# Optimization experiments

Measured on AMD Instinct MI355X. Metric: run time of the kernel, lower is better.

The kernel has to match this reference:

```python
import jax, jax.numpy as jnp
import numpy as np

B, N, D, H = 256, 40, 256, 256      # molecules, atoms/molecule, pc_hidden, pred_hidden
nS, nC, nB = 40, 5, 5               # n_SYMBOLS, n_FORMAL_CHARGES, n_BOND_TYPES
NEG_SLOPE = 0.01                    # F.leaky_relu default


def _lrelu(x):
    return jnp.where(x >= 0, x, NEG_SLOPE * x)


def setup_inputs() -> dict:
    key = jax.random.key(0)
    ks = jax.random.split(key, 7)
    def w(k, shape, fan_in):
        return jax.random.normal(k, shape, jnp.float32) / np.float32(np.sqrt(fan_in))
    return {
        "yhat": jax.random.normal(ks[0], (B, N, D), jnp.float32),
        "Ws1": w(ks[1], (D, H), D),      "bs1": jnp.zeros((H,), jnp.float32),
        "Ws2": w(ks[2], (H, nS), H),     "bs2": jnp.zeros((nS,), jnp.float32),
        "Wc1": w(ks[3], (D, H), D),      "bc1": jnp.zeros((H,), jnp.float32),
        "Wc2": w(ks[4], (H, nC), H),     "bc2": jnp.zeros((nC,), jnp.float32),
        "Wb1": w(ks[5], (2 * D, H), 2 * D), "bb1": jnp.zeros((H,), jnp.float32),
        "Wb2": w(ks[6], (H, nB), H),     "bb2": jnp.zeros((nB,), jnp.float32),
    }


def reference(yhat, Ws1, bs1, Ws2, bs2, Wc1, bc1, Wc2, bc2, Wb1, bb1, Wb2, bb2):
    # Per-atom symbol / charge heads (2-layer MLP with leaky_relu)
    symbols = _lrelu(yhat @ Ws1 + bs1) @ Ws2 + bs2          # [B, N, nS]
    charges = _lrelu(yhat @ Wc1 + bc1) @ Wc2 + bc2          # [B, N, nC]

    # Pairwise bond head: concat(x_i, x_j) @ Wb1 == x_i @ Wb1[:D] + x_j @ Wb1[D:]
    # (avoids materializing the [B, N, N, 2D] concat tensor)
    p1 = yhat @ Wb1[:D]                                      # [B, N, H]
    p2 = yhat @ Wb1[D:]                                      # [B, N, H]
    h = _lrelu(p1[:, :, None, :] + p2[:, None, :, :] + bb1)  # [B, N, N, H]
    bonds = h @ Wb2 + bb2                                    # [B, N, N, nB]
    bonds = bonds + jnp.swapaxes(bonds, 1, 2)                # symmetrize (i,j)+(j,i)

    return (symbols.reshape(-1, nS),
            charges.reshape(-1, nC),
            bonds.reshape(-1, nB))
```

## Files before the change

kernel.cpp:

```cpp
#include <hip/hip_runtime.h>
#include <hip/hip_bf16.h>

typedef unsigned short u16;
typedef __attribute__((ext_vector_type(4))) int   int4v;
typedef __attribute__((ext_vector_type(4))) unsigned int uint4v;
typedef __attribute__((ext_vector_type(4))) unsigned short ushort4v;
typedef __attribute__((ext_vector_type(4))) float floatx4;
typedef __attribute__((ext_vector_type(8))) short bf16x8;
typedef _Float16 half8 __attribute__((ext_vector_type(8)));
typedef _Float16 half2v __attribute__((ext_vector_type(2)));

#define LRELU_NS 0.01f
#define SK 264

__device__ __forceinline__ float bitsToF(unsigned int b) {
    union { unsigned int u; float f; } v; v.u = b << 16; return v.f;
}
__device__ __forceinline__ u16 f2bf(float f) {
    __hip_bfloat16 h = __float2bfloat16(f);
    return *reinterpret_cast<u16*>(&h);
}
__device__ __forceinline__ float lrelu(float v) {
    return fmaxf(v, LRELU_NS * v);
}
__device__ __forceinline__ u16 ldW(const void* p, int i, int isF32) {
    return isF32 ? f2bf(((const float*)p)[i]) : ((const u16*)p)[i];
}
__device__ __forceinline__ float ldF(const void* p, int i, int isF32) {
    return isF32 ? ((const float*)p)[i]
                 : bitsToF((unsigned int)((const u16*)p)[i]);
}
__device__ __forceinline__ u16 f2h_bits(float f) {
    union { _Float16 h; u16 u; } v; v.h = (_Float16)f; return v.u;
}
__device__ __forceinline__ u16 ldWh(const void* p, int i, int isF32) {
    float f = isF32 ? ((const float*)p)[i]
                    : bitsToF((unsigned int)((const u16*)p)[i]);
    return f2h_bits(f);
}
__device__ __forceinline__ half2v u2h2(unsigned int x) {
    union { unsigned int u; half2v h; } v; v.u = x; return v.h;
}
__device__ __forceinline__ unsigned int h22u(half2v x) {
    union { half2v h; unsigned int u; } v; v.h = x; return v.u;
}

__device__ __forceinline__ int computeIsF32(const u16* y, int* cnt, int t) {
    if (t == 0) *cnt = 0;
    __syncthreads();
    if (t < 256) {
        u16 v = y[2 * t];
        int e = (v >> 7) & 0xFF;
        if (v == 0 || (e >= 96 && e < 160)) atomicAdd(cnt, 1);
    }
    __syncthreads();
    return (*cnt < 192) ? 1 : 0;
}

__global__ __launch_bounds__(256) void pack_kernel(
    const void* __restrict__ yhat,
    const void* __restrict__ Ws1, const void* __restrict__ Wc1,
    const void* __restrict__ Wb1, const void* __restrict__ Ws2,
    const void* __restrict__ Wc2,
    const void* __restrict__ bs1, const void* __restrict__ bc1,
    const void* __restrict__ bb1, const void* __restrict__ bs2,
    const void* __restrict__ bc2, const void* __restrict__ bb2,
    u16* __restrict__ WallT, u16* __restrict__ W2T, float* __restrict__ biasF)
{
    __shared__ int fcnt;
    const int bid = blockIdx.x, t = threadIdx.x;
    const int isF32 = computeIsF32((const u16*)yhat, &fcnt, t);
    if (bid < 64) {
        __shared__ u16 tile[64][65];
        const int c0 = (bid & 15) * 64;
        const int k0 = (bid >> 4) * 64;
        const void* src; int coff; int roff = 0;
        if (c0 < 256)      { src = Ws1; coff = c0; }
        else if (c0 < 512) { src = Wc1; coff = c0 - 256; }
        else if (c0 < 768) { src = Wb1; coff = c0 - 512; }
        else               { src = Wb1; coff = c0 - 768; roff = 256; }
        const int cc = t & 63, kk0 = t >> 6;
        #pragma unroll
        for (int i = 0; i < 16; ++i) {
            int kk = kk0 + i * 4;
            tile[kk][cc] = ldW(src, (k0 + kk + roff) * 256 + coff + cc, isF32);
        }
        __syncthreads();
        const int kk2 = t & 63, cc0 = t >> 6;
        #pragma unroll
        for (int i = 0; i < 16; ++i) {
            int cc2 = cc0 + i * 4;
            WallT[(c0 + cc2) * 256 + (k0 + kk2)] = tile[kk2][cc2];
        }
    } else if (bid < 128) {
        int e2 = (bid - 64) * 256 + t;
        int c = e2 >> 8, k = e2 & 255;
        u16 v = 0;
        if (c < 40)                 v = ldW(Ws2, k * 40 + c, isF32);
        else if (c >= 48 && c < 53) v = ldW(Wc2, k * 5 + (c - 48), isF32);
        W2T[c * 256 + k] = v;
    } else {
        int idx = (bid - 128) * 256 + t;
        float v = 0.f;
        if (idx < 256)       v = ldF(bs1, idx, isF32);
        else if (idx < 512)  v = ldF(bc1, idx - 256, isF32);
        else if (idx < 768)  v = ldF(bb1, idx - 512, isF32);
        else if (idx < 808)  v = ldF(bs2, idx - 768, isF32);
        else if (idx < 813)  v = ldF(bc2, idx - 808, isF32);
        else if (idx >= 816 && idx < 821) v = ldF(bb2, idx - 816, isF32);
        biasF[idx] = v;
    }
}

union SharedHB {
    struct { u16 Xs[64 * SK]; u16 Hb[64 * SK]; } hd;
    struct { u16 Xm[48 * SK]; u16 P1L[48 * SK]; u16 P2L[48 * SK];
             u16 WsB[5 * 264]; } bd;
};

__global__ __launch_bounds__(512) void fused_kernel(
    const void* __restrict__ Xv, const u16* __restrict__ WallT,
    const u16* __restrict__ W2T, const void* __restrict__ Wb2,
    const float* __restrict__ biasF, void* __restrict__ outv)
{
    __shared__ SharedHB sh;
    __shared__ int fcnt;
    const int t = threadIdx.x;
    const int bid = blockIdx.x;
    const int isF32 = computeIsF32((const u16*)Xv, &fcnt, t);

    const int w = t >> 6, l = t & 63;
    const int ml = l & 15, kq = l >> 4, r0 = kq * 4;

    if (bid < 512) {
        const int b = bid >> 1;
        const int h = bid & 1;

        if (isF32) {
            const floatx4* __restrict__ src = (const floatx4*)((const float*)Xv + b * 10240);
            #pragma unroll
            for (int s = 0; s < 5; ++s) {
                int cid = t + s * 512;
                int row = cid >> 6, ch = cid & 63;
                floatx4 f = src[cid];
                ushort4v u;
                u[0] = f2bf(f[0]); u[1] = f2bf(f[1]); u[2] = f2bf(f[2]); u[3] = f2bf(f[3]);
                *(ushort4v*)&sh.bd.Xm[row * SK + ch * 4] = u;
            }
            {
                int row = 40 + (t >> 6), ch = t & 63;
                ushort4v z = {0, 0, 0, 0};
                *(ushort4v*)&sh.bd.Xm[row * SK + ch * 4] = z;
            }
        } else {
            const int4v* __restrict__ src = (const int4v*)((const u16*)Xv + b * 10240);
            #pragma unroll
            for (int s = 0; s < 3; ++s) {
                int cid = t + s * 512;
                int row = cid >> 5, ch = cid & 31;
                if (cid < 1280) *(int4v*)&sh.bd.Xm[row * SK + ch * 8] = src[cid];
                else { int4v z = {0, 0, 0, 0}; *(int4v*)&sh.bd.Xm[row * SK + ch * 8] = z; }
            }
        }
        #pragma unroll
        for (int s = 0; s < 3; ++s) {
            int e2 = t + s * 512;
            if (e2 < 1280) {
                int c = e2 >> 8, k = e2 & 255;
                sh.bd.WsB[c * 264 + k] = ldWh(Wb2, k * 5 + c, isF32);
            }
        }
        __syncthreads();

        for (int n = 0; n < 4; ++n) {
            const int gc = (w + 8 * n) * 16 + ml;
            floatx4 acc[3] = {};
            #pragma unroll
            for (int ks = 0; ks < 8; ++ks) {
                const int k0 = ks * 32 + kq * 8;
                bf16x8 bf = *(const bf16x8*)&WallT[(512 + gc) * 256 + k0];
                #pragma unroll
                for (int i = 0; i < 3; ++i) {
                    bf16x8 a = *(const bf16x8*)&sh.bd.Xm[(i * 16 + ml) * SK + k0];
                    acc[i] = __builtin_amdgcn_mfma_f32_16x16x32_bf16(a, bf, acc[i], 0, 0, 0);
                }
            }
            u16* dst = (gc < 256) ? sh.bd.P1L : sh.bd.P2L;
            const int col = gc & 255;
            const float bias = (gc < 256) ? biasF[512 + gc] : 0.f;
            #pragma unroll
            for (int i = 0; i < 3; ++i)
                #pragma unroll
                for (int r = 0; r < 4; ++r)
                    dst[(i * 16 + r0 + r) * SK + col] = f2h_bits(acc[i][r] + bias);
        }
        __syncthreads();

        const int sel = (ml < 5) ? ml : 4;
        half8 wf[8];
        #pragma unroll
        for (int ks = 0; ks < 8; ++ks)
            wf[ks] = *(const half8*)&sh.bd.WsB[sel * 264 + ks * 32 + kq * 8];
        const float b2x2 = 2.f * biasF[816 + ml];
        const _Float16 c001 = (_Float16)0.01f;

        constexpr int mT[11]  = {0, 0, 0, 1, 1, 1, 2, 2, 3, 3, 4};
        constexpr int jtT[11] = {0, 1, 2, 0, 1, 2, 1, 2, 1, 2, 2};
        #pragma unroll
        for (int idx = 0; idx < 11; ++idx) {
            if ((idx & 1) != h) continue;
            const int m = mT[idx], jt = jtT[idx];
            const int i = w + 8 * m;
            const bool diag = (jt == (i >> 4));
            floatx4 acc = {};
            #pragma unroll
            for (int ks = 0; ks < 8; ++ks) {
                const int k0 = ks * 32 + kq * 8;
                const uint4v a1 = *(const uint4v*)&sh.bd.P1L[i * SK + k0];
                const uint4v a2 = *(const uint4v*)&sh.bd.P2L[i * SK + k0];
                const uint4v b1 = *(const uint4v*)&sh.bd.P1L[(jt * 16 + ml) * SK + k0];
                const uint4v b2 = *(const uint4v*)&sh.bd.P2L[(jt * 16 + ml) * SK + k0];
                union { unsigned int u[4]; half8 v; } af;
                #pragma unroll
                for (int d = 0; d < 4; ++d) {
                    const half2v tF = u2h2(a1[d]) + u2h2(b2[d]);
                    const half2v tB = u2h2(b1[d]) + u2h2(a2[d]);
                    const half2v lF = __builtin_elementwise_max(tF, tF * c001);
                    const half2v lB = __builtin_elementwise_max(tB, tB * c001);
                    af.u[d] = h22u(lF + lB);
                }
                acc = __builtin_amdgcn_mfma_f32_16x16x32_f16(af.v, wf[ks], acc, 0, 0, 0);
            }
            if (ml < 5) {
                #pragma unroll
                for (int r = 0; r < 4; ++r) {
                    const int j = jt * 16 + r0 + r;
                    if (j < 40 && (!diag || j >= i)) {
                        const float v = acc[r] + b2x2;
                        const int o1 = 460800 + (b * 1600 + i * 40 + j) * 5 + ml;
                        if (isF32) ((float*)outv)[o1] = v;
                        else ((__hip_bfloat16*)outv)[o1] = __float2bfloat16(v);
                        if (!diag || j > i) {
                            const int o2 = 460800 + (b * 1600 + j * 40 + i) * 5 + ml;
                            if (isF32) ((float*)outv)[o2] = v;
                            else ((__hip_bfloat16*)outv)[o2] = __float2bfloat16(v);
                        }
                    }
                }
            }
        }
    } else {
        const int hb = bid - 512;
        const int bm0 = (hb % 160) * 64;
        const int head = hb / 160;

        if (isF32) {
            const floatx4* __restrict__ src = (const floatx4*)((const float*)Xv + bm0 * 256);
            #pragma unroll
            for (int s = 0; s < 8; ++s) {
                int cid = t + s * 512;
                int row = cid >> 6, ch = cid & 63;
                floatx4 f = src[cid];
                ushort4v u;
                u[0] = f2bf(f[0]); u[1] = f2bf(f[1]); u[2] = f2bf(f[2]); u[3] = f2bf(f[3]);
                *(ushort4v*)&sh.hd.Xs[row * SK + ch * 4] = u;
            }
        } else {
            const int4v* __restrict__ src = (const int4v*)((const u16*)Xv + bm0 * 256);
            #pragma unroll
            for (int s = 0; s < 4; ++s) {
                int cid = t + s * 512;
                int row = cid >> 5, ch = cid & 31;
                *(int4v*)&sh.hd.Xs[row * SK + ch * 8] = src[cid];
            }
        }
        __syncthreads();

        #pragma unroll
        for (int n = 0; n < 2; ++n) {
            const int ct = w + 8 * n;
            floatx4 acc[4] = {};
            #pragma unroll
            for (int ks = 0; ks < 8; ++ks) {
                const int k0 = ks * 32 + kq * 8;
                bf16x8 bf = *(const bf16x8*)&WallT[(head * 256 + ct * 16 + ml) * 256 + k0];
                #pragma unroll
                for (int mt = 0; mt < 4; ++mt) {
                    bf16x8 a = *(const bf16x8*)&sh.hd.Xs[(mt * 16 + ml) * SK + k0];
                    acc[mt] = __builtin_amdgcn_mfma_f32_16x16x32_bf16(a, bf, acc[mt], 0, 0, 0);
                }
            }
            const int col = ct * 16 + ml;
            const float bias = biasF[head * 256 + col];
            #pragma unroll
            for (int mt = 0; mt < 4; ++mt)
                #pragma unroll
                for (int r = 0; r < 4; ++r)
                    sh.hd.Hb[(mt * 16 + r0 + r) * SK + col] = f2bf(lrelu(acc[mt][r] + bias));
        }
        __syncthreads();

        if (w < 4) {
            const int nct = (head == 0) ? 3 : 1;
            const int c0  = (head == 0) ? 0 : 48;
            floatx4 acc2[3] = {};
            #pragma unroll
            for (int ks = 0; ks < 8; ++ks) {
                const int k0 = ks * 32 + kq * 8;
                bf16x8 a = *(const bf16x8*)&sh.hd.Hb[(w * 16 + ml) * SK + k0];
                #pragma unroll
                for (int j = 0; j < 3; ++j) {
                    if (j < nct) {
                        bf16x8 bf = *(const bf16x8*)&W2T[(c0 + j * 16 + ml) * 256 + k0];
                        acc2[j] = __builtin_amdgcn_mfma_f32_16x16x32_bf16(a, bf, acc2[j], 0, 0, 0);
                    }
                }
            }
            #pragma unroll
            for (int j = 0; j < 3; ++j) {
                if (j < nct) {
                    const int col = j * 16 + ml;
                    const int lim = (head == 0) ? 40 : 5;
                    if (col < lim) {
                        const float bias = biasF[(head == 0 ? 768 : 808) + col];
                        #pragma unroll
                        for (int r = 0; r < 4; ++r) {
                            const int row = bm0 + w * 16 + r0 + r;
                            const int o = (head == 0) ? row * 40 + col
                                                      : 409600 + row * 5 + col;
                            const float v = acc2[j][r] + bias;
                            if (isF32) ((float*)outv)[o] = v;
                            else ((__hip_bfloat16*)outv)[o] = __float2bfloat16(v);
                        }
                    }
                }
            }
        }
    }
}

extern "C" void kernel_launch(void* const* d_in, const int* in_sizes, int n_in,
                              void* d_out, int out_size, void* d_ws, size_t ws_size,
                              hipStream_t stream)
{
    const void* yhat = d_in[0];
    const void* Ws1  = d_in[1];
    const void* bs1  = d_in[2];
    const void* Ws2  = d_in[3];
    const void* bs2  = d_in[4];
    const void* Wc1  = d_in[5];
    const void* bc1  = d_in[6];
    const void* Wc2  = d_in[7];
    const void* bc2  = d_in[8];
    const void* Wb1  = d_in[9];
    const void* bb1  = d_in[10];
    const void* Wb2  = d_in[11];
    const void* bb2  = d_in[12];

    char* wsb = (char*)d_ws;
    float* biasF = (float*)(wsb + 4096);
    u16*   W2T   = (u16*)(wsb + 8192);
    u16*   WallT = (u16*)(wsb + 40960);

    pack_kernel<<<132, 256, 0, stream>>>(yhat, Ws1, Wc1, Wb1, Ws2, Wc2,
                                         bs1, bc1, bb1, bs2, bc2, bb2,
                                         WallT, W2T, biasF);
    fused_kernel<<<832, 512, 0, stream>>>(yhat, WallT, W2T, Wb2, biasF, d_out);
}
```

Before: 133.8 us.

## Alias LDS buffers across phases to shrink shared memory and raise occupancy

Overlays the input tile with the P1/hidden buffers in shared memory. The MFMA results are held in packed registers, a barrier is inserted, and only then are they written into the aliased region. This reduces LDS per block (the bond path drops from about 3 tiles to 2, the heads path from 2 to 1), so more workgroups can be resident per CU, and launch_bounds now requests 6. The cost is an extra __syncthreads per path and more live registers, which could cause spills under the tighter register budget.

```diff
diff --git a/kernel.cpp b/kernel.cpp
--- a/kernel.cpp
+++ b/kernel.cpp
@@ -113,12 +113,17 @@
 }
 
 union SharedHB {
-    struct { u16 Xs[64 * SK]; u16 Hb[64 * SK]; } hd;
-    struct { u16 Xm[48 * SK]; u16 P1L[48 * SK]; u16 P2L[48 * SK];
-             u16 WsB[5 * 264]; } bd;
+    struct {
+        union { u16 Xm[48 * SK]; u16 P1L[48 * SK]; } a;
+        u16 P2L[48 * SK];
+        u16 WsB[5 * 264];
+    } bd;
+    struct {
+        union { u16 Xs[64 * SK]; u16 Hb[64 * SK]; } x;
+    } hd;
 };
 
-__global__ __launch_bounds__(512) void fused_kernel(
+__global__ __launch_bounds__(512, 6) void fused_kernel(
     const void* __restrict__ Xv, const u16* __restrict__ WallT,
     const u16* __restrict__ W2T, const void* __restrict__ Wb2,
     const float* __restrict__ biasF, void* __restrict__ outv)
@@ -145,12 +150,12 @@
                 floatx4 f = src[cid];
                 ushort4v u;
                 u[0] = f2bf(f[0]); u[1] = f2bf(f[1]); u[2] = f2bf(f[2]); u[3] = f2bf(f[3]);
-                *(ushort4v*)&sh.bd.Xm[row * SK + ch * 4] = u;
+                *(ushort4v*)&sh.bd.a.Xm[row * SK + ch * 4] = u;
             }
             {
                 int row = 40 + (t >> 6), ch = t & 63;
                 ushort4v z = {0, 0, 0, 0};
-                *(ushort4v*)&sh.bd.Xm[row * SK + ch * 4] = z;
+                *(ushort4v*)&sh.bd.a.Xm[row * SK + ch * 4] = z;
             }
         } else {
             const int4v* __restrict__ src = (const int4v*)((const u16*)Xv + b * 10240);
@@ -158,8 +163,8 @@
             for (int s = 0; s < 3; ++s) {
                 int cid = t + s * 512;
                 int row = cid >> 5, ch = cid & 31;
-                if (cid < 1280) *(int4v*)&sh.bd.Xm[row * SK + ch * 8] = src[cid];
-                else { int4v z = {0, 0, 0, 0}; *(int4v*)&sh.bd.Xm[row * SK + ch * 8] = z; }
+                if (cid < 1280) *(int4v*)&sh.bd.a.Xm[row * SK + ch * 8] = src[cid];
+                else { int4v z = {0, 0, 0, 0}; *(int4v*)&sh.bd.a.Xm[row * SK + ch * 8] = z; }
             }
         }
         #pragma unroll
@@ -172,6 +177,8 @@
         }
         __syncthreads();
 
+        unsigned int pH[24];
+        #pragma unroll
         for (int n = 0; n < 4; ++n) {
             const int gc = (w + 8 * n) * 16 + ml;
             floatx4 acc[3] = {};
@@ -181,18 +188,37 @@
                 bf16x8 bf = *(const bf16x8*)&WallT[(512 + gc) * 256 + k0];
                 #pragma unroll
                 for (int i = 0; i < 3; ++i) {
-                    bf16x8 a = *(const bf16x8*)&sh.bd.Xm[(i * 16 + ml) * SK + k0];
+                    bf16x8 a = *(const bf16x8*)&sh.bd.a.Xm[(i * 16 + ml) * SK + k0];
                     acc[i] = __builtin_amdgcn_mfma_f32_16x16x32_bf16(a, bf, acc[i], 0, 0, 0);
                 }
             }
-            u16* dst = (gc < 256) ? sh.bd.P1L : sh.bd.P2L;
+            const float bias = (gc < 256) ? biasF[512 + gc] : 0.f;
+            #pragma unroll
+            for (int i = 0; i < 3; ++i) {
+                const unsigned int h0 = f2h_bits(acc[i][0] + bias);
+                const unsigned int h1 = f2h_bits(acc[i][1] + bias);
+                const unsigned int h2 = f2h_bits(acc[i][2] + bias);
+                const unsigned int h3 = f2h_bits(acc[i][3] + bias);
+                pH[n * 6 + i * 2 + 0] = h0 | (h1 << 16);
+                pH[n * 6 + i * 2 + 1] = h2 | (h3 << 16);
+            }
+        }
+        __syncthreads();
+
+        #pragma unroll
+        for (int n = 0; n < 4; ++n) {
+            const int gc = (w + 8 * n) * 16 + ml;
+            u16* dst = (gc < 256) ? sh.bd.a.P1L : sh.bd.P2L;
             const int col = gc & 255;
-            const float bias = (gc < 256) ? biasF[512 + gc] : 0.f;
-            #pragma unroll
-            for (int i = 0; i < 3; ++i)
-                #pragma unroll
-                for (int r = 0; r < 4; ++r)
-                    dst[(i * 16 + r0 + r) * SK + col] = f2h_bits(acc[i][r] + bias);
+            #pragma unroll
+            for (int i = 0; i < 3; ++i) {
+                const unsigned int p0 = pH[n * 6 + i * 2 + 0];
+                const unsigned int p1 = pH[n * 6 + i * 2 + 1];
+                dst[(i * 16 + r0 + 0) * SK + col] = (u16)(p0 & 0xffff);
+                dst[(i * 16 + r0 + 1) * SK + col] = (u16)(p0 >> 16);
+                dst[(i * 16 + r0 + 2) * SK + col] = (u16)(p1 & 0xffff);
+                dst[(i * 16 + r0 + 3) * SK + col] = (u16)(p1 >> 16);
+            }
         }
         __syncthreads();
 
@@ -216,9 +242,9 @@
             #pragma unroll
             for (int ks = 0; ks < 8; ++ks) {
                 const int k0 = ks * 32 + kq * 8;
-                const uint4v a1 = *(const uint4v*)&sh.bd.P1L[i * SK + k0];
+                const uint4v a1 = *(const uint4v*)&sh.bd.a.P1L[i * SK + k0];
                 const uint4v a2 = *(const uint4v*)&sh.bd.P2L[i * SK + k0];
-                const uint4v b1 = *(const uint4v*)&sh.bd.P1L[(jt * 16 + ml) * SK + k0];
+                const uint4v b1 = *(const uint4v*)&sh.bd.a.P1L[(jt * 16 + ml) * SK + k0];
                 const uint4v b2 = *(const uint4v*)&sh.bd.P2L[(jt * 16 + ml) * SK + k0];
                 union { unsigned int u[4]; half8 v; } af;
                 #pragma unroll
@@ -263,7 +289,7 @@
                 floatx4 f = src[cid];
                 ushort4v u;
                 u[0] = f2bf(f[0]); u[1] = f2bf(f[1]); u[2] = f2bf(f[2]); u[3] = f2bf(f[3]);
-                *(ushort4v*)&sh.hd.Xs[row * SK + ch * 4] = u;
+                *(ushort4v*)&sh.hd.x.Xs[row * SK + ch * 4] = u;
             }
         } else {
             const int4v* __restrict__ src = (const int4v*)((const u16*)Xv + bm0 * 256);
@@ -271,11 +297,12 @@
             for (int s = 0; s < 4; ++s) {
                 int cid = t + s * 512;
                 int row = cid >> 5, ch = cid & 31;
-                *(int4v*)&sh.hd.Xs[row * SK + ch * 8] = src[cid];
-            }
-        }
-        __syncthreads();
-
+                *(int4v*)&sh.hd.x.Xs[row * SK + ch * 8] = src[cid];
+            }
+        }
+        __syncthreads();
+
+        unsigned int hH[16];
         #pragma unroll
         for (int n = 0; n < 2; ++n) {
             const int ct = w + 8 * n;
@@ -286,17 +313,36 @@
                 bf16x8 bf = *(const bf16x8*)&WallT[(head * 256 + ct * 16 + ml) * 256 + k0];
                 #pragma unroll
                 for (int mt = 0; mt < 4; ++mt) {
-                    bf16x8 a = *(const bf16x8*)&sh.hd.Xs[(mt * 16 + ml) * SK + k0];
+                    bf16x8 a = *(const bf16x8*)&sh.hd.x.Xs[(mt * 16 + ml) * SK + k0];
                     acc[mt] = __builtin_amdgcn_mfma_f32_16x16x32_bf16(a, bf, acc[mt], 0, 0, 0);
                 }
             }
             const int col = ct * 16 + ml;
             const float bias = biasF[head * 256 + col];
             #pragma unroll
-            for (int mt = 0; mt < 4; ++mt)
-                #pragma unroll
-                for (int r = 0; r < 4; ++r)
-                    sh.hd.Hb[(mt * 16 + r0 + r) * SK + col] = f2bf(lrelu(acc[mt][r] + bias));
+            for (int mt = 0; mt < 4; ++mt) {
+                const unsigned int b0 = f2bf(lrelu(acc[mt][0] + bias));
+                const unsigned int b1 = f2bf(lrelu(acc[mt][1] + bias));
+                const unsigned int b2 = f2bf(lrelu(acc[mt][2] + bias));
+                const unsigned int b3 = f2bf(lrelu(acc[mt][3] + bias));
+                hH[n * 8 + mt * 2 + 0] = b0 | (b1 << 16);
+                hH[n * 8 + mt * 2 + 1] = b2 | (b3 << 16);
+            }
+        }
+        __syncthreads();
+
+        #pragma unroll
+        for (int n = 0; n < 2; ++n) {
+            const int col = (w + 8 * n) * 16 + ml;
+            #pragma unroll
+            for (int mt = 0; mt < 4; ++mt) {
+                const unsigned int p0 = hH[n * 8 + mt * 2 + 0];
+                const unsigned int p1 = hH[n * 8 + mt * 2 + 1];
+                sh.hd.x.Hb[(mt * 16 + r0 + 0) * SK + col] = (u16)(p0 & 0xffff);
+                sh.hd.x.Hb[(mt * 16 + r0 + 1) * SK + col] = (u16)(p0 >> 16);
+                sh.hd.x.Hb[(mt * 16 + r0 + 2) * SK + col] = (u16)(p1 & 0xffff);
+                sh.hd.x.Hb[(mt * 16 + r0 + 3) * SK + col] = (u16)(p1 >> 16);
+            }
         }
         __syncthreads();
 
@@ -307,7 +353,7 @@
             #pragma unroll
             for (int ks = 0; ks < 8; ++ks) {
                 const int k0 = ks * 32 + kq * 8;
-                bf16x8 a = *(const bf16x8*)&sh.hd.Hb[(w * 16 + ml) * SK + k0];
+                bf16x8 a = *(const bf16x8*)&sh.hd.x.Hb[(w * 16 + ml) * SK + k0];
                 #pragma unroll
                 for (int j = 0; j < 3; ++j) {
                     if (j < nct) {
```

New measurement: 169.3 us. +26.6%, slower.
